# Performance work log

Measured on AMD Instinct MI355X. Metric: run time of the kernel, lower is better.

The kernel has to match this reference:

```python
import jax, jax.numpy as jnp
import numpy as np

INPUT_DIM = 512
MIX = 32
HID = 96
B, T = 256, 512


def setup_inputs() -> dict:
    key = jax.random.key(0)
    ks = jax.random.split(key, 8)
    s = lambda fan_in: 1.0 / np.sqrt(fan_in)
    x = jax.random.normal(ks[0], (B, T, INPUT_DIM), dtype=jnp.float32)
    # mix: Linear(INPUT_DIM, MIX, bias=False) -> weight [MIX, INPUT_DIM]
    W_mix = jax.random.uniform(ks[1], (MIX, INPUT_DIM), jnp.float32, -s(INPUT_DIM), s(INPUT_DIM))
    # GRU layer 0 weights, PyTorch layout: [3H, in], [3H, H], biases [3H]
    W_ih = jax.random.uniform(ks[2], (3 * HID, MIX), jnp.float32, -s(HID), s(HID))
    W_hh = jax.random.uniform(ks[3], (3 * HID, HID), jnp.float32, -s(HID), s(HID))
    b_ih = jax.random.uniform(ks[4], (3 * HID,), jnp.float32, -s(HID), s(HID))
    b_hh = jax.random.uniform(ks[5], (3 * HID,), jnp.float32, -s(HID), s(HID))
    # head: Linear(HID, MIX)
    W_head = jax.random.uniform(ks[6], (MIX, HID), jnp.float32, -s(HID), s(HID))
    b_head = jax.random.uniform(ks[7], (MIX,), jnp.float32, -s(HID), s(HID))
    return {"x": x, "W_mix": W_mix, "W_ih": W_ih, "W_hh": W_hh,
            "b_ih": b_ih, "b_hh": b_hh, "W_head": W_head, "b_head": b_head}


def _gru_last(z, W_ih, W_hh, b_ih, b_hh):
    # z: [B, T, MIX]. Precompute all input-side gate pre-activations: [T, B, 3H]
    gx = jnp.einsum('btm,gm->tbg', z, W_ih) + b_ih
    h0 = jnp.zeros((z.shape[0], HID), dtype=z.dtype)

    def step(h, gx_t):
        gh = h @ W_hh.T + b_hh  # [B, 3H]
        xr, xz, xn = jnp.split(gx_t, 3, axis=-1)
        hr, hz, hn = jnp.split(gh, 3, axis=-1)
        r = jax.nn.sigmoid(xr + hr)
        u = jax.nn.sigmoid(xz + hz)
        n = jnp.tanh(xn + r * hn)
        h_new = (1.0 - u) * n + u * h
        return h_new, None

    h_last, _ = jax.lax.scan(step, h0, gx)
    return h_last  # [B, HID]


def reference(x, W_mix, W_ih, W_hh, b_ih, b_hh, W_head, b_head):
    z = x @ W_mix.T                       # [B, T, MIX]
    last = _gru_last(z, W_ih, W_hh, b_ih, b_hh)  # [B, HID]
    z_next = last @ W_head.T + b_head     # [B, MIX]
    y_next = z_next @ W_mix               # [B, INPUT_DIM] (tied weights)
    return y_next
```

## Files before the change

kernel.cpp:

```cpp
#include <hip/hip_runtime.h>

#define IDIM 512
#define MIXD 32
#define HID 96
#define BB 256
#define TT 512
#define TROWS 32

typedef float f32x2 __attribute__((ext_vector_type(2)));
typedef float f32x4 __attribute__((ext_vector_type(4)));

#define EXP2(x) __builtin_amdgcn_exp2f(x)

template <int CTRL>
__device__ __forceinline__ float dpp_shl_add(float x) {
    int m = __builtin_amdgcn_update_dpp(0, __float_as_int(x), CTRL, 0xf, 0xf, true);
    return x + __int_as_float(m);
}
__device__ __forceinline__ float octet_reduce_lane0(float x) {
    x = dpp_shl_add<0x104>(x);
    x = dpp_shl_add<0x102>(x);
    x = dpp_shl_add<0x101>(x);
    return x;
}
__device__ __forceinline__ void pinv(f32x2 &v) { asm volatile("" : "+v"(v)); }
__device__ __forceinline__ void pinf(float &v) { asm volatile("" : "+v"(v)); }

__global__ __launch_bounds__(256) void k_mix(const float* __restrict__ x,
                                             const float* __restrict__ Wmix,
                                             float* __restrict__ z) {
    __shared__ __align__(16) float sx[TROWS * IDIM];
    const int tid = threadIdx.x;
    const int mg = tid >> 3, ks = tid & 7;

    f32x2 w[32];
    #pragma unroll
    for (int i = 0; i < 16; ++i) {
        const int cj = (i + 2 * ks) & 15;
        f32x4 v = *(const f32x4*)(Wmix + (size_t)mg * IDIM + ks * 64 + cj * 4);
        w[2*i] = v.xy; w[2*i+1] = v.zw;
    }

    const size_t rowbase = (size_t)blockIdx.x * 256;
    const float* xb = x + rowbase * IDIM;

    f32x4 st[16];
    #pragma unroll
    for (int i = 0; i < 16; ++i)
        st[i] = *(const f32x4*)(xb + (size_t)(tid + 256 * i) * 4);

    for (int t = 0; t < 8; ++t) {
        #pragma unroll
        for (int i = 0; i < 16; ++i)
            *(f32x4*)(&sx[(tid + 256 * i) * 4]) = st[i];
        __syncthreads();

        if (t + 1 < 8) {
            const float* xn = xb + (size_t)(t + 1) * TROWS * IDIM;
            #pragma unroll
            for (int i = 0; i < 16; ++i)
                st[i] = *(const f32x4*)(xn + (size_t)(tid + 256 * i) * 4);
        }

        float* zp = z + (rowbase + (size_t)t * TROWS) * MIXD + mg;
        for (int r = 0; r < TROWS; ++r) {
            const float* rp = sx + r * IDIM + ks * 64;
            f32x2 acc = {0.f, 0.f};
            #pragma unroll
            for (int i = 0; i < 16; ++i) {
                f32x4 v = *(const f32x4*)(rp + ((i + 2 * ks) & 15) * 4);
                acc = __builtin_elementwise_fma(w[2*i],   v.xy, acc);
                acc = __builtin_elementwise_fma(w[2*i+1], v.zw, acc);
            }
            float s = octet_reduce_lane0(acc.x + acc.y);
            if (ks == 0) zp[(size_t)r * MIXD] = s;
        }
        __syncthreads();
    }
}

__global__ __launch_bounds__(256, 1) void k_scan(const float* __restrict__ z,
                                                 const float* __restrict__ Wih,
                                                 const float* __restrict__ Whh,
                                                 const float* __restrict__ bih,
                                                 const float* __restrict__ bhh,
                                                 const float* __restrict__ Whead,
                                                 const float* __restrict__ bhead,
                                                 const float* __restrict__ Wmix,
                                                 float* __restrict__ y) {
    const int b   = blockIdx.x;
    const int tid = threadIdx.x;
    const int j0  = tid >> 3;
    const int o   = tid & 7;
    const float L  = 1.4426950408889634f;
    const float L2 = 2.8853900817779268f;

    __shared__ __align__(16) float sz[256 * MIXD];
    __shared__ __align__(16) float shp[2][HID];
    __shared__ __align__(16) float szn[MIXD];

    f32x2 whr[3][6], whu[3][6], whn[3][6], wir[3][2], wiu[3][2], win[3][2];
    float br[3], bu[3], bxn[3], bhn[3];
    #pragma unroll
    for (int i = 0; i < 3; ++i) {
        const int j = j0 + 32 * i;
        #pragma unroll
        for (int c = 0; c < 3; ++c) {
            f32x4 v = *(const f32x4*)(Whh + (size_t)(j        ) * HID + o * 12 + c * 4);
            v *= L;  whr[i][2*c] = v.xy; whr[i][2*c+1] = v.zw;
        }
        #pragma unroll
        for (int c = 0; c < 3; ++c) {
            f32x4 v = *(const f32x4*)(Whh + (size_t)(j +   HID) * HID + o * 12 + c * 4);
            v *= L;  whu[i][2*c] = v.xy; whu[i][2*c+1] = v.zw;
        }
        #pragma unroll
        for (int c = 0; c < 3; ++c) {
            f32x4 v = *(const f32x4*)(Whh + (size_t)(j + 2*HID) * HID + o * 12 + c * 4);
            v *= L2; whn[i][2*c] = v.xy; whn[i][2*c+1] = v.zw;
        }
        {
            f32x4 v = *(const f32x4*)(Wih + (size_t)(j        ) * MIXD + o * 4);
            v *= L;  wir[i][0] = v.xy; wir[i][1] = v.zw;
        }
        {
            f32x4 v = *(const f32x4*)(Wih + (size_t)(j +   HID) * MIXD + o * 4);
            v *= L;  wiu[i][0] = v.xy; wiu[i][1] = v.zw;
        }
        {
            f32x4 v = *(const f32x4*)(Wih + (size_t)(j + 2*HID) * MIXD + o * 4);
            v *= L2; win[i][0] = v.xy; win[i][1] = v.zw;
        }
        br[i]  = (o == 0) ? L  * (bih[j]       + bhh[j])       : 0.f;
        bu[i]  = (o == 0) ? L  * (bih[j + HID] + bhh[j + HID]) : 0.f;
        bxn[i] = (o == 0) ? L2 * bih[j + 2*HID] : 0.f;
        bhn[i] = (o == 0) ? L2 * bhh[j + 2*HID] : 0.f;
    }

    float hown[3] = {0.f, 0.f, 0.f};
    if (tid < HID) shp[0][tid] = 0.f;

    const f32x4* zb4 = (const f32x4*)(z + (size_t)b * TT * MIXD);
    f32x4* sz4 = (f32x4*)sz;

    for (int c = 0; c < TT / 256; ++c) {
        #pragma unroll
        for (int i = 0; i < 8; ++i)
            sz4[tid + 256 * i] = zb4[c * 2048 + tid + 256 * i];
        __syncthreads();

        for (int tt = 0; tt < 256; ++tt) {
            #pragma unroll
            for (int i = 0; i < 3; ++i) {
                #pragma unroll
                for (int k = 0; k < 6; ++k) { pinv(whr[i][k]); pinv(whu[i][k]); pinv(whn[i][k]); }
                pinv(wir[i][0]); pinv(wir[i][1]);
                pinv(wiu[i][0]); pinv(wiu[i][1]);
                pinv(win[i][0]); pinv(win[i][1]);
                pinf(br[i]); pinf(bu[i]); pinf(bxn[i]); pinf(bhn[i]);
            }

            const int t = (c << 8) + tt;
            const float* hr = shp[t & 1];
            float*       hw = shp[(t + 1) & 1];

            const f32x4 z4 = *(const f32x4*)(sz + tt * MIXD + o * 4);
            const f32x4 h0 = *(const f32x4*)(hr + o * 12);
            const f32x4 h1 = *(const f32x4*)(hr + o * 12 + 4);
            const f32x4 h2 = *(const f32x4*)(hr + o * 12 + 8);
            const f32x2 hh[6] = { h0.xy, h0.zw, h1.xy, h1.zw, h2.xy, h2.zw };

            float hv[3];
            #pragma unroll
            for (int i = 0; i < 3; ++i) {
                f32x2 aR  = {br[i],  0.f}, aU  = {bu[i],  0.f};
                f32x2 aXN = {bxn[i], 0.f}, aHN = {bhn[i], 0.f};

                aR  = __builtin_elementwise_fma(wir[i][0], z4.xy, aR);
                aR  = __builtin_elementwise_fma(wir[i][1], z4.zw, aR);
                aU  = __builtin_elementwise_fma(wiu[i][0], z4.xy, aU);
                aU  = __builtin_elementwise_fma(wiu[i][1], z4.zw, aU);
                aXN = __builtin_elementwise_fma(win[i][0], z4.xy, aXN);
                aXN = __builtin_elementwise_fma(win[i][1], z4.zw, aXN);

                #pragma unroll
                for (int k = 0; k < 6; ++k) {
                    aR  = __builtin_elementwise_fma(whr[i][k], hh[k], aR);
                    aU  = __builtin_elementwise_fma(whu[i][k], hh[k], aU);
                    aHN = __builtin_elementwise_fma(whn[i][k], hh[k], aHN);
                }

                float sR  = octet_reduce_lane0(aR.x  + aR.y);
                float sU  = octet_reduce_lane0(aU.x  + aU.y);
                float sXN = octet_reduce_lane0(aXN.x + aXN.y);
                float sHN = octet_reduce_lane0(aHN.x + aHN.y);

                float r = __builtin_amdgcn_rcpf(1.f + EXP2(-sR));
                float u = __builtin_amdgcn_rcpf(1.f + EXP2(-sU));
                float n = 1.f - 2.f * __builtin_amdgcn_rcpf(1.f + EXP2(sXN + r * sHN));
                hv[i] = u * (hown[i] - n) + n;
                hown[i] = hv[i];
            }
            if (o == 0) {
                hw[j0]      = hv[0];
                hw[j0 + 32] = hv[1];
                hw[j0 + 64] = hv[2];
            }
            __syncthreads();
        }
    }

    if (tid < MIXD) {
        const float* h = shp[0];
        float a0 = 0.f, a1 = 0.f, a2 = 0.f, a3 = 0.f;
        #pragma unroll
        for (int kc = 0; kc < HID / 4; ++kc) {
            f32x4 wv = *(const f32x4*)(Whead + (size_t)tid * HID + kc * 4);
            f32x4 hv4 = *(const f32x4*)(h + kc * 4);
            a0 += wv.x * hv4.x; a1 += wv.y * hv4.y;
            a2 += wv.z * hv4.z; a3 += wv.w * hv4.w;
        }
        szn[tid] = bhead[tid] + ((a0 + a1) + (a2 + a3));
    }
    __syncthreads();
    #pragma unroll
    for (int rep = 0; rep < 2; ++rep) {
        const int col = tid + 256 * rep;
        float acc = 0.f;
        #pragma unroll
        for (int m = 0; m < MIXD; ++m)
            acc += szn[m] * Wmix[(size_t)m * IDIM + col];
        y[(size_t)b * IDIM + col] = acc;
    }
}

extern "C" void kernel_launch(void* const* d_in, const int* in_sizes, int n_in,
                              void* d_out, int out_size, void* d_ws, size_t ws_size,
                              hipStream_t stream) {
    const float* x     = (const float*)d_in[0];
    const float* Wmix  = (const float*)d_in[1];
    const float* Wih   = (const float*)d_in[2];
    const float* Whh   = (const float*)d_in[3];
    const float* bih   = (const float*)d_in[4];
    const float* bhh   = (const float*)d_in[5];
    const float* Whead = (const float*)d_in[6];
    const float* bhead = (const float*)d_in[7];
    float* out = (float*)d_out;

    float* z = (float*)d_ws;

    k_mix <<<512, 256, 0, stream>>>(x, Wmix, z);
    k_scan<<<BB,  256, 0, stream>>>(z, Wih, Whh, bih, bhh, Whead, bhead, Wmix, out);
}
```

Measured before the change: 369.9 us.

## Process two batch rows per scan block to interleave independent recurrences

Each k_scan block now advances two batch sequences at once, sharing the register-resident weights and interleaving two independent FMA/reduce/transcendental chains per timestep. Grid size halves from 256 to 128 blocks, so half as many CUs are used, but each step gets twice the instruction-level parallelism to hide DPP and exp/rcp latency. The register pinning asm barriers are also removed, and shared memory for z chunks doubles.

```diff
diff --git a/kernel.cpp b/kernel.cpp
--- a/kernel.cpp
+++ b/kernel.cpp
@@ -23,8 +23,6 @@
     x = dpp_shl_add<0x101>(x);
     return x;
 }
-__device__ __forceinline__ void pinv(f32x2 &v) { asm volatile("" : "+v"(v)); }
-__device__ __forceinline__ void pinf(float &v) { asm volatile("" : "+v"(v)); }
 
 __global__ __launch_bounds__(256) void k_mix(const float* __restrict__ x,
                                              const float* __restrict__ Wmix,
@@ -88,16 +86,16 @@
                                                  const float* __restrict__ bhead,
                                                  const float* __restrict__ Wmix,
                                                  float* __restrict__ y) {
-    const int b   = blockIdx.x;
+    const int b0  = blockIdx.x * 2;
     const int tid = threadIdx.x;
     const int j0  = tid >> 3;
     const int o   = tid & 7;
     const float L  = 1.4426950408889634f;
     const float L2 = 2.8853900817779268f;
 
-    __shared__ __align__(16) float sz[256 * MIXD];
-    __shared__ __align__(16) float shp[2][HID];
-    __shared__ __align__(16) float szn[MIXD];
+    __shared__ __align__(16) float sz[2][256 * MIXD];
+    __shared__ __align__(16) float shp[2][2][HID];
+    __shared__ __align__(16) float szn[2][MIXD];
 
     f32x2 whr[3][6], whu[3][6], whn[3][6], wir[3][2], wiu[3][2], win[3][2];
     float br[3], bu[3], bxn[3], bhn[3];
@@ -137,100 +135,126 @@
         bhn[i] = (o == 0) ? L2 * bhh[j + 2*HID] : 0.f;
     }
 
-    float hown[3] = {0.f, 0.f, 0.f};
-    if (tid < HID) shp[0][tid] = 0.f;
-
-    const f32x4* zb4 = (const f32x4*)(z + (size_t)b * TT * MIXD);
-    f32x4* sz4 = (f32x4*)sz;
+    float hown[3][2] = {{0.f,0.f},{0.f,0.f},{0.f,0.f}};
+    if (tid < HID) { shp[0][0][tid] = 0.f; shp[1][0][tid] = 0.f; }
+
+    const f32x4* zb0 = (const f32x4*)(z + (size_t)(b0    ) * TT * MIXD);
+    const f32x4* zb1 = (const f32x4*)(z + (size_t)(b0 + 1) * TT * MIXD);
+    f32x4* sz40 = (f32x4*)sz[0];
+    f32x4* sz41 = (f32x4*)sz[1];
 
     for (int c = 0; c < TT / 256; ++c) {
         #pragma unroll
-        for (int i = 0; i < 8; ++i)
-            sz4[tid + 256 * i] = zb4[c * 2048 + tid + 256 * i];
+        for (int i = 0; i < 8; ++i) {
+            sz40[tid + 256 * i] = zb0[c * 2048 + tid + 256 * i];
+            sz41[tid + 256 * i] = zb1[c * 2048 + tid + 256 * i];
+        }
         __syncthreads();
 
         for (int tt = 0; tt < 256; ++tt) {
+            const int t = (c << 8) + tt;
+            const int pr = t & 1, pw = (t + 1) & 1;
+
+            const f32x4 z4a = *(const f32x4*)(sz[0] + tt * MIXD + o * 4);
+            const f32x4 z4b = *(const f32x4*)(sz[1] + tt * MIXD + o * 4);
+            const float* hra = shp[0][pr];
+            const float* hrb = shp[1][pr];
+            const f32x4 ha0 = *(const f32x4*)(hra + o * 12);
+            const f32x4 ha1 = *(const f32x4*)(hra + o * 12 + 4);
+            const f32x4 ha2 = *(const f32x4*)(hra + o * 12 + 8);
+            const f32x4 hb0 = *(const f32x4*)(hrb + o * 12);
+            const f32x4 hb1 = *(const f32x4*)(hrb + o * 12 + 4);
+            const f32x4 hb2 = *(const f32x4*)(hrb + o * 12 + 8);
+            const f32x2 hha[6] = { ha0.xy, ha0.zw, ha1.xy, ha1.zw, ha2.xy, ha2.zw };
+            const f32x2 hhb[6] = { hb0.xy, hb0.zw, hb1.xy, hb1.zw, hb2.xy, hb2.zw };
+
+            float hv[3][2];
             #pragma unroll
             for (int i = 0; i < 3; ++i) {
-                #pragma unroll
-                for (int k = 0; k < 6; ++k) { pinv(whr[i][k]); pinv(whu[i][k]); pinv(whn[i][k]); }
-                pinv(wir[i][0]); pinv(wir[i][1]);
-                pinv(wiu[i][0]); pinv(wiu[i][1]);
-                pinv(win[i][0]); pinv(win[i][1]);
-                pinf(br[i]); pinf(bu[i]); pinf(bxn[i]); pinf(bhn[i]);
-            }
-
-            const int t = (c << 8) + tt;
-            const float* hr = shp[t & 1];
-            float*       hw = shp[(t + 1) & 1];
-
-            const f32x4 z4 = *(const f32x4*)(sz + tt * MIXD + o * 4);
-            const f32x4 h0 = *(const f32x4*)(hr + o * 12);
-            const f32x4 h1 = *(const f32x4*)(hr + o * 12 + 4);
-            const f32x4 h2 = *(const f32x4*)(hr + o * 12 + 8);
-            const f32x2 hh[6] = { h0.xy, h0.zw, h1.xy, h1.zw, h2.xy, h2.zw };
-
-            float hv[3];
-            #pragma unroll
-            for (int i = 0; i < 3; ++i) {
-                f32x2 aR  = {br[i],  0.f}, aU  = {bu[i],  0.f};
-                f32x2 aXN = {bxn[i], 0.f}, aHN = {bhn[i], 0.f};
-
-                aR  = __builtin_elementwise_fma(wir[i][0], z4.xy, aR);
-                aR  = __builtin_elementwise_fma(wir[i][1], z4.zw, aR);
-                aU  = __builtin_elementwise_fma(wiu[i][0], z4.xy, aU);
-                aU  = __builtin_elementwise_fma(wiu[i][1], z4.zw, aU);
-                aXN = __builtin_elementwise_fma(win[i][0], z4.xy, aXN);
-                aXN = __builtin_elementwise_fma(win[i][1], z4.zw, aXN);
+                f32x2 aRa  = {br[i],  0.f}, aUa  = {bu[i],  0.f};
+                f32x2 aXNa = {bxn[i], 0.f}, aHNa = {bhn[i], 0.f};
+                f32x2 aRb  = {br[i],  0.f}, aUb  = {bu[i],  0.f};
+                f32x2 aXNb = {bxn[i], 0.f}, aHNb = {bhn[i], 0.f};
+
+                aRa  = __builtin_elementwise_fma(wir[i][0], z4a.xy, aRa);
+                aRb  = __builtin_elementwise_fma(wir[i][0], z4b.xy, aRb);
+                aRa  = __builtin_elementwise_fma(wir[i][1], z4a.zw, aRa);
+                aRb  = __builtin_elementwise_fma(wir[i][1], z4b.zw, aRb);
+                aUa  = __builtin_elementwise_fma(wiu[i][0], z4a.xy, aUa);
+                aUb  = __builtin_elementwise_fma(wiu[i][0], z4b.xy, aUb);
+                aUa  = __builtin_elementwise_fma(wiu[i][1], z4a.zw, aUa);
+                aUb  = __builtin_elementwise_fma(wiu[i][1], z4b.zw, aUb);
+                aXNa = __builtin_elementwise_fma(win[i][0], z4a.xy, aXNa);
+                aXNb = __builtin_elementwise_fma(win[i][0], z4b.xy, aXNb);
+                aXNa = __builtin_elementwise_fma(win[i][1], z4a.zw, aXNa);
+                aXNb = __builtin_elementwise_fma(win[i][1], z4b.zw, aXNb);
 
                 #pragma unroll
                 for (int k = 0; k < 6; ++k) {
-                    aR  = __builtin_elementwise_fma(whr[i][k], hh[k], aR);
-                    aU  = __builtin_elementwise_fma(whu[i][k], hh[k], aU);
-                    aHN = __builtin_elementwise_fma(whn[i][k], hh[k], aHN);
+                    aRa  = __builtin_elementwise_fma(whr[i][k], hha[k], aRa);
+                    aRb  = __builtin_elementwise_fma(whr[i][k], hhb[k], aRb);
+                    aUa  = __builtin_elementwise_fma(whu[i][k], hha[k], aUa);
+                    aUb  = __builtin_elementwise_fma(whu[i][k], hhb[k], aUb);
+                    aHNa = __builtin_elementwise_fma(whn[i][k], hha[k], aHNa);
+                    aHNb = __builtin_elementwise_fma(whn[i][k], hhb[k], aHNb);
                 }
 
-                float sR  = octet_reduce_lane0(aR.x  + aR.y);
-                float sU  = octet_reduce_lane0(aU.x  + aU.y);
-                float sXN = octet_reduce_lane0(aXN.x + aXN.y);
-                float sHN = octet_reduce_lane0(aHN.x + aHN.y);
-
-                float r = __builtin_amdgcn_rcpf(1.f + EXP2(-sR));
-                float u = __builtin_amdgcn_rcpf(1.f + EXP2(-sU));
-                float n = 1.f - 2.f * __builtin_amdgcn_rcpf(1.f + EXP2(sXN + r * sHN));
-                hv[i] = u * (hown[i] - n) + n;
-                hown[i] = hv[i];
+                float sRa  = octet_reduce_lane0(aRa.x  + aRa.y);
+                float sRb  = octet_reduce_lane0(aRb.x  + aRb.y);
+                float sUa  = octet_reduce_lane0(aUa.x  + aUa.y);
+                float sUb  = octet_reduce_lane0(aUb.x  + aUb.y);
+                float sXNa = octet_reduce_lane0(aXNa.x + aXNa.y);
+                float sXNb = octet_reduce_lane0(aXNb.x + aXNb.y);
+                float sHNa = octet_reduce_lane0(aHNa.x + aHNa.y);
+                float sHNb = octet_reduce_lane0(aHNb.x + aHNb.y);
+
+                float ra = __builtin_amdgcn_rcpf(1.f + EXP2(-sRa));
+                float rb = __builtin_amdgcn_rcpf(1.f + EXP2(-sRb));
+                float ua = __builtin_amdgcn_rcpf(1.f + EXP2(-sUa));
+                float ub = __builtin_amdgcn_rcpf(1.f + EXP2(-sUb));
+                float na = 1.f - 2.f * __builtin_amdgcn_rcpf(1.f + EXP2(sXNa + ra * sHNa));
+                float nb = 1.f - 2.f * __builtin_amdgcn_rcpf(1.f + EXP2(sXNb + rb * sHNb));
+                hv[i][0] = ua * (hown[i][0] - na) + na;
+                hv[i][1] = ub * (hown[i][1] - nb) + nb;
+                hown[i][0] = hv[i][0];
+                hown[i][1] = hv[i][1];
             }
             if (o == 0) {
-                hw[j0]      = hv[0];
-                hw[j0 + 32] = hv[1];
-                hw[j0 + 64] = hv[2];
+                float* hwa = shp[0][pw];
+                float* hwb = shp[1][pw];
+                hwa[j0]      = hv[0][0];  hwb[j0]      = hv[0][1];
+                hwa[j0 + 32] = hv[1][0];  hwb[j0 + 32] = hv[1][1];
+                hwa[j0 + 64] = hv[2][0];  hwb[j0 + 64] = hv[2][1];
             }
             __syncthreads();
         }
     }
 
-    if (tid < MIXD) {
-        const float* h = shp[0];
+    if (tid < 64) {
+        const int bb = tid >> 5, m = tid & 31;
+        const float* h = shp[bb][0];
         float a0 = 0.f, a1 = 0.f, a2 = 0.f, a3 = 0.f;
         #pragma unroll
         for (int kc = 0; kc < HID / 4; ++kc) {
-            f32x4 wv = *(const f32x4*)(Whead + (size_t)tid * HID + kc * 4);
+            f32x4 wv = *(const f32x4*)(Whead + (size_t)m * HID + kc * 4);
             f32x4 hv4 = *(const f32x4*)(h + kc * 4);
             a0 += wv.x * hv4.x; a1 += wv.y * hv4.y;
             a2 += wv.z * hv4.z; a3 += wv.w * hv4.w;
         }
-        szn[tid] = bhead[tid] + ((a0 + a1) + (a2 + a3));
+        szn[bb][m] = bhead[m] + ((a0 + a1) + (a2 + a3));
     }
     __syncthreads();
     #pragma unroll
-    for (int rep = 0; rep < 2; ++rep) {
-        const int col = tid + 256 * rep;
-        float acc = 0.f;
-        #pragma unroll
-        for (int m = 0; m < MIXD; ++m)
-            acc += szn[m] * Wmix[(size_t)m * IDIM + col];
-        y[(size_t)b * IDIM + col] = acc;
+    for (int bb = 0; bb < 2; ++bb) {
+        #pragma unroll
+        for (int r2 = 0; r2 < 2; ++r2) {
+            const int col = tid + 256 * r2;
+            float acc = 0.f;
+            #pragma unroll
+            for (int m = 0; m < MIXD; ++m)
+                acc += szn[bb][m] * Wmix[(size_t)m * IDIM + col];
+            y[(size_t)(b0 + bb) * IDIM + col] = acc;
+        }
     }
 }
 
@@ -250,5 +274,5 @@
     float* z = (float*)d_ws;
 
     k_mix <<<512, 256, 0, stream>>>(x, Wmix, z);
-    k_scan<<<BB,  256, 0, stream>>>(z, Wih, Whh, bih, bhh, Whead, bhead, Wmix, out);
-}
+    k_scan<<<BB / 2, 256, 0, stream>>>(z, Wih, Whh, bih, bhh, Whead, bhead, Wmix, out);
+}
```

New measurement: 571.9 us. 54.6% more time.

## Pad mix LDS rows, compute two outputs per thread, split GRU FMA chains, prefetch z

Applied to the files above, without the earlier changes.

In the mix kernel, shared-memory rows are padded to 516 floats, and each 16-lane group now computes two output channels over 32-element slices with a 16-lane DPP reduction. This is meant to cut LDS bank conflicts and get more reuse per loaded x vector. In the scan kernel, the empty-asm register pinning is removed, each gate dot product is split into two independent FMA chains to shorten dependency latency, and the next step's z vector is loaded before the barrier. Dropping the pinning could let the compiler rematerialize or spill weights, and the extra accumulators raise register pressure.

```diff
diff --git a/kernel.cpp b/kernel.cpp
--- a/kernel.cpp
+++ b/kernel.cpp
@@ -6,6 +6,7 @@
 #define BB 256
 #define TT 512
 #define TROWS 32
+#define SROW 516
 
 typedef float f32x2 __attribute__((ext_vector_type(2)));
 typedef float f32x4 __attribute__((ext_vector_type(4)));
@@ -23,22 +24,29 @@
     x = dpp_shl_add<0x101>(x);
     return x;
 }
-__device__ __forceinline__ void pinv(f32x2 &v) { asm volatile("" : "+v"(v)); }
-__device__ __forceinline__ void pinf(float &v) { asm volatile("" : "+v"(v)); }
+__device__ __forceinline__ float red16(float x) {
+    x = dpp_shl_add<0x108>(x);
+    x = dpp_shl_add<0x104>(x);
+    x = dpp_shl_add<0x102>(x);
+    x = dpp_shl_add<0x101>(x);
+    return x;
+}
 
 __global__ __launch_bounds__(256) void k_mix(const float* __restrict__ x,
                                              const float* __restrict__ Wmix,
                                              float* __restrict__ z) {
-    __shared__ __align__(16) float sx[TROWS * IDIM];
+    __shared__ __align__(16) float sx[TROWS * SROW];
     const int tid = threadIdx.x;
-    const int mg = tid >> 3, ks = tid & 7;
-
-    f32x2 w[32];
-    #pragma unroll
-    for (int i = 0; i < 16; ++i) {
-        const int cj = (i + 2 * ks) & 15;
-        f32x4 v = *(const f32x4*)(Wmix + (size_t)mg * IDIM + ks * 64 + cj * 4);
-        w[2*i] = v.xy; w[2*i+1] = v.zw;
+    const int mg = tid >> 4, ks = tid & 15;
+
+    f32x2 w0[16], w1[16];
+    #pragma unroll
+    for (int i = 0; i < 8; ++i) {
+        const int cj = (i + ks) & 7;
+        f32x4 v0 = *(const f32x4*)(Wmix + (size_t)(2 * mg)     * IDIM + ks * 32 + cj * 4);
+        f32x4 v1 = *(const f32x4*)(Wmix + (size_t)(2 * mg + 1) * IDIM + ks * 32 + cj * 4);
+        w0[2*i] = v0.xy; w0[2*i+1] = v0.zw;
+        w1[2*i] = v1.xy; w1[2*i+1] = v1.zw;
     }
 
     const size_t rowbase = (size_t)blockIdx.x * 256;
@@ -51,8 +59,10 @@
 
     for (int t = 0; t < 8; ++t) {
         #pragma unroll
-        for (int i = 0; i < 16; ++i)
-            *(f32x4*)(&sx[(tid + 256 * i) * 4]) = st[i];
+        for (int i = 0; i < 16; ++i) {
+            const int v = tid + 256 * i, r = v >> 7, c = v & 127;
+            *(f32x4*)(&sx[r * SROW + c * 4]) = st[i];
+        }
         __syncthreads();
 
         if (t + 1 < 8) {
@@ -62,18 +72,24 @@
                 st[i] = *(const f32x4*)(xn + (size_t)(tid + 256 * i) * 4);
         }
 
-        float* zp = z + (rowbase + (size_t)t * TROWS) * MIXD + mg;
+        float* zp = z + (rowbase + (size_t)t * TROWS) * MIXD + 2 * mg;
         for (int r = 0; r < TROWS; ++r) {
-            const float* rp = sx + r * IDIM + ks * 64;
-            f32x2 acc = {0.f, 0.f};
+            const float* rp = sx + r * SROW + ks * 32;
+            f32x2 a0 = {0.f, 0.f}, a1 = {0.f, 0.f};
             #pragma unroll
-            for (int i = 0; i < 16; ++i) {
-                f32x4 v = *(const f32x4*)(rp + ((i + 2 * ks) & 15) * 4);
-                acc = __builtin_elementwise_fma(w[2*i],   v.xy, acc);
-                acc = __builtin_elementwise_fma(w[2*i+1], v.zw, acc);
-            }
-            float s = octet_reduce_lane0(acc.x + acc.y);
-            if (ks == 0) zp[(size_t)r * MIXD] = s;
+            for (int i = 0; i < 8; ++i) {
+                f32x4 v = *(const f32x4*)(rp + ((i + ks) & 7) * 4);
+                a0 = __builtin_elementwise_fma(w0[2*i],   v.xy, a0);
+                a0 = __builtin_elementwise_fma(w0[2*i+1], v.zw, a0);
+                a1 = __builtin_elementwise_fma(w1[2*i],   v.xy, a1);
+                a1 = __builtin_elementwise_fma(w1[2*i+1], v.zw, a1);
+            }
+            float s0 = red16(a0.x + a0.y);
+            float s1 = red16(a1.x + a1.y);
+            if (ks == 0) {
+                f32x2 o2 = { s0, s1 };
+                *(f32x2*)(zp + (size_t)r * MIXD) = o2;
+            }
         }
         __syncthreads();
     }
@@ -149,22 +165,12 @@
             sz4[tid + 256 * i] = zb4[c * 2048 + tid + 256 * i];
         __syncthreads();
 
+        f32x4 z4 = *(const f32x4*)(sz + 0 * MIXD + o * 4);
         for (int tt = 0; tt < 256; ++tt) {
-            #pragma unroll
-            for (int i = 0; i < 3; ++i) {
-                #pragma unroll
-                for (int k = 0; k < 6; ++k) { pinv(whr[i][k]); pinv(whu[i][k]); pinv(whn[i][k]); }
-                pinv(wir[i][0]); pinv(wir[i][1]);
-                pinv(wiu[i][0]); pinv(wiu[i][1]);
-                pinv(win[i][0]); pinv(win[i][1]);
-                pinf(br[i]); pinf(bu[i]); pinf(bxn[i]); pinf(bhn[i]);
-            }
-
             const int t = (c << 8) + tt;
             const float* hr = shp[t & 1];
             float*       hw = shp[(t + 1) & 1];
 
-            const f32x4 z4 = *(const f32x4*)(sz + tt * MIXD + o * 4);
             const f32x4 h0 = *(const f32x4*)(hr + o * 12);
             const f32x4 h1 = *(const f32x4*)(hr + o * 12 + 4);
             const f32x4 h2 = *(const f32x4*)(hr + o * 12 + 8);
@@ -173,27 +179,32 @@
             float hv[3];
             #pragma unroll
             for (int i = 0; i < 3; ++i) {
-                f32x2 aR  = {br[i],  0.f}, aU  = {bu[i],  0.f};
-                f32x2 aXN = {bxn[i], 0.f}, aHN = {bhn[i], 0.f};
+                f32x2 aR  = {br[i],  0.f}, aR2  = {0.f, 0.f};
+                f32x2 aU  = {bu[i],  0.f}, aU2  = {0.f, 0.f};
+                f32x2 aXN = {bxn[i], 0.f};
+                f32x2 aHN = {bhn[i], 0.f}, aHN2 = {0.f, 0.f};
 
                 aR  = __builtin_elementwise_fma(wir[i][0], z4.xy, aR);
-                aR  = __builtin_elementwise_fma(wir[i][1], z4.zw, aR);
+                aR2 = __builtin_elementwise_fma(wir[i][1], z4.zw, aR2);
                 aU  = __builtin_elementwise_fma(wiu[i][0], z4.xy, aU);
-                aU  = __builtin_elementwise_fma(wiu[i][1], z4.zw, aU);
+                aU2 = __builtin_elementwise_fma(wiu[i][1], z4.zw, aU2);
                 aXN = __builtin_elementwise_fma(win[i][0], z4.xy, aXN);
                 aXN = __builtin_elementwise_fma(win[i][1], z4.zw, aXN);
 
                 #pragma unroll
-                for (int k = 0; k < 6; ++k) {
-                    aR  = __builtin_elementwise_fma(whr[i][k], hh[k], aR);
-                    aU  = __builtin_elementwise_fma(whu[i][k], hh[k], aU);
-                    aHN = __builtin_elementwise_fma(whn[i][k], hh[k], aHN);
+                for (int k = 0; k < 3; ++k) {
+                    aR   = __builtin_elementwise_fma(whr[i][k],   hh[k],   aR);
+                    aR2  = __builtin_elementwise_fma(whr[i][k+3], hh[k+3], aR2);
+                    aU   = __builtin_elementwise_fma(whu[i][k],   hh[k],   aU);
+                    aU2  = __builtin_elementwise_fma(whu[i][k+3], hh[k+3], aU2);
+                    aHN  = __builtin_elementwise_fma(whn[i][k],   hh[k],   aHN);
+                    aHN2 = __builtin_elementwise_fma(whn[i][k+3], hh[k+3], aHN2);
                 }
 
-                float sR  = octet_reduce_lane0(aR.x  + aR.y);
-                float sU  = octet_reduce_lane0(aU.x  + aU.y);
+                float sR  = octet_reduce_lane0((aR.x  + aR.y)  + (aR2.x  + aR2.y));
+                float sU  = octet_reduce_lane0((aU.x  + aU.y)  + (aU2.x  + aU2.y));
                 float sXN = octet_reduce_lane0(aXN.x + aXN.y);
-                float sHN = octet_reduce_lane0(aHN.x + aHN.y);
+                float sHN = octet_reduce_lane0((aHN.x + aHN.y) + (aHN2.x + aHN2.y));
 
                 float r = __builtin_amdgcn_rcpf(1.f + EXP2(-sR));
                 float u = __builtin_amdgcn_rcpf(1.f + EXP2(-sU));
@@ -206,7 +217,10 @@
                 hw[j0 + 32] = hv[1];
                 hw[j0 + 64] = hv[2];
             }
+            f32x4 z4n = z4;
+            if (tt + 1 < 256) z4n = *(const f32x4*)(sz + (tt + 1) * MIXD + o * 4);
             __syncthreads();
+            z4 = z4n;
         }
     }
 
```

Result: slower. 385.8 us (+4.3%).
